# Optimization experiments

Measured on AMD Instinct MI355X. Metric: run time of the kernel, lower is better.

## Reference

```python
import jax, jax.numpy as jnp
import numpy as np

NEG_INF = -2.0**32 + 1

def positional_encoding(seq_len, dim):
    pos = np.arange(seq_len)[:, None].astype(np.float32)
    i = np.arange(dim)[None, :]
    angle_rads = pos / np.power(10000.0, 2 * (i // 2) / np.float32(dim))
    angle_rads[:, 0::2] = np.sin(angle_rads[:, 0::2])
    angle_rads[:, 1::2] = np.cos(angle_rads[:, 1::2])
    return jnp.asarray(angle_rads[None, ...], dtype=jnp.float32)  # [1, S, dim]

def setup_inputs() -> dict:
    key = jax.random.key(0)
    kq, kk, kv, km, kw = jax.random.split(key, 5)
    B, S, D = 32, 1024, 256
    return {
        'q': jax.random.normal(kq, (B, S, D), dtype=jnp.float32),
        'k': jax.random.normal(kk, (B, S, D), dtype=jnp.float32),
        'v': jax.random.normal(kv, (B, S, D), dtype=jnp.float32),
        'mask': jax.random.randint(km, (B, S), 0, 2, dtype=jnp.int32),
        'W': jax.random.uniform(kw, (D, D), dtype=jnp.float32),
    }

def reference(q, k, v, mask, W):
    B, S, D = q.shape
    pe = positional_encoding(S, D)  # [1, S, D]
    q = q + pe
    k = k + pe
    q = jax.nn.relu(jnp.matmul(q, W))
    k = jax.nn.relu(jnp.matmul(k, W))
    # scaled attention logits [B, S, S]
    logits = jnp.einsum('bqd,bkd->bqk', q, k) / jnp.sqrt(jnp.float32(D))
    m = mask[:, None, :]  # [B, 1, S], broadcasts over query dim
    logits = jnp.where(m == 0, jnp.float32(NEG_INF), logits)
    attn = jax.nn.softmax(logits, axis=-1)
    out = jnp.matmul(attn, v)          # [B, S, D]
    return jnp.mean(out, axis=1)       # [B, D]
```

## Files before the change

### kernel.cpp

```cpp
#include <hip/hip_runtime.h>

typedef float    f32x4  __attribute__((ext_vector_type(4)));
typedef float    f32x16 __attribute__((ext_vector_type(16)));
typedef _Float16 h16x8  __attribute__((ext_vector_type(8)));

#define NB 32
#define NS 1024
#define ND 256
#define NK 640
#define NEGINF (-4.2949673e9f)

__device__ __forceinline__ f32x4 mfmah(h16x8 a, h16x8 b, f32x4 c) {
    return __builtin_amdgcn_mfma_f32_16x16x32_f16(a, b, c, 0, 0, 0);
}

#define PIN(x)  asm volatile("" : "+v"(x))
#define WAITV8  asm volatile("s_waitcnt vmcnt(8)" ::: "memory")
#define WAITV0  asm volatile("s_waitcnt vmcnt(0)" ::: "memory")
#define LGKM0   asm volatile("s_waitcnt lgkmcnt(0)" ::: "memory")
#define SCHEDB  __builtin_amdgcn_sched_barrier(0)

template <typename T>
__device__ __forceinline__ void gload16(const T* g, void* l) {
    __builtin_amdgcn_global_load_lds(
        (const __attribute__((address_space(1))) void*)g,
        (__attribute__((address_space(3))) void*)l, 16, 0, 0);
}


__global__ void setup_kernel(const float* __restrict__ W, float* __restrict__ pe,
                             _Float16* __restrict__ wtt,
                             _Float16* __restrict__ wtt32) {
    int t = threadIdx.x;
    int bid = blockIdx.x;
    if (bid < 1024) {
        int s = bid, d = t;
        float f = __builtin_exp2f(-(float)(d >> 1) * 0.10381025296523007f);
        float ang = (float)s * f;
        pe[s * ND + d] = (d & 1) ? cosf(ang) : sinf(ang);
    } else if (bid < 1280) {
        int idx = (bid - 1024) * 256 + t;
        int n = idx >> 8, d = idx & 255;
        int bn = n >> 7, wn = (n >> 6) & 1, j = (n >> 4) & 3, nr = n & 15;
        int kk = d >> 5, dg = (d >> 3) & 3, e = d & 7;
        int lane = dg * 16 + nr;
        size_t off = (size_t)((((bn * 8 + kk) * 2 + wn) * 4 + j)) * 512 + lane * 8 + e;
        wtt[off] = (_Float16)W[(size_t)d * ND + n];
    } else {
        int idx = (bid - 1280) * 256 + t;
        int n = idx >> 8, d = idx & 255;
        int lane = (n & 31) + ((d >> 3) & 1) * 32;
        size_t off = (size_t)((n >> 5) * 16 + (d >> 4)) * 512 + lane * 8 + (d & 7);
        wtt32[off] = (_Float16)W[(size_t)d * ND + n];
    }
}

__global__ __launch_bounds__(256) void scan_kernel(const int* __restrict__ mask,
                                                   int* __restrict__ idxl,
                                                   int* __restrict__ cnt) {
    __shared__ int sb[256];
    int b = blockIdx.x, t = threadIdx.x;
    int m[4], psum = 0;
    #pragma unroll
    for (int e = 0; e < 4; ++e) {
        m[e] = (mask[b * 1024 + t * 4 + e] != 0) ? 1 : 0;
        psum += m[e];
    }
    sb[t] = psum;
    __syncthreads();
    #pragma unroll
    for (int off = 1; off < 256; off <<= 1) {
        int v = (t >= off) ? sb[t - off] : 0;
        __syncthreads();
        sb[t] += v;
        __syncthreads();
    }
    int excl = sb[t] - psum;
    int total = sb[255];
    int pos = excl;
    #pragma unroll
    for (int e = 0; e < 4; ++e) {
        if (m[e]) {
            if (pos < NK) idxl[b * NK + pos] = t * 4 + e;
            ++pos;
        }
    }
    if (t == 0) cnt[b] = (total > NK) ? NK : total;
    for (int p = total + t; p < NK; p += 256) idxl[b * NK + p] = 0;
}

__global__ __launch_bounds__(256, 3) void proj_kernel(
    const float* __restrict__ k, const float* __restrict__ pe,
    const _Float16* __restrict__ wtt, const int* __restrict__ idxl,
    _Float16* __restrict__ kph) {
    __shared__ __align__(16) _Float16 la[2][128][40];
    __shared__ __align__(16) _Float16 lb[2][4096];
    int t = threadIdx.x;
    int wg = blockIdx.x;
    int swz = (wg & 7) * 40 + (wg >> 3);
    int bb = swz >> 1, bn = swz & 1;
    int phase = bb & 7;
    int lane = t & 63, wid = t >> 6;
    int wm = wid >> 1, wn = wid & 1;
    int lr = lane & 15, lg = lane >> 4;

    int r0 = t >> 2, qtr0 = (t & 3) * 8;
    int r1 = 64 + (t >> 2), qtr1 = qtr0;
    int b = bb / 5, c = bb - (bb / 5) * 5;
    int o0 = idxl[b * NK + c * 128 + r0];
    int o1 = idxl[b * NK + c * 128 + r1];
    const float* aRow0 = k + ((size_t)b * 1024 + o0) * ND;
    const float* aRow1 = k + ((size_t)b * 1024 + o1) * ND;
    const float* pRow0 = pe + (size_t)o0 * ND;
    const float* pRow1 = pe + (size_t)o1 * ND;
    long destbase = (long)b * NK + c * 128;
    const _Float16* bsrc = wtt + (size_t)bn * 32768;

    f32x4 acc[4][4];
    #pragma unroll
    for (int i = 0; i < 4; ++i)
        #pragma unroll
        for (int j = 0; j < 4; ++j) acc[i][j] = (f32x4){0.f, 0.f, 0.f, 0.f};

    f32x4 ax[2][4], ap[2][4];
#define ISSUE_A(s, cc)                                                        \
    {                                                                         \
        int db_ = (cc) * 32;                                                  \
        ax[s][0] = *(const f32x4*)(aRow0 + db_ + qtr0);                       \
        ax[s][1] = *(const f32x4*)(aRow0 + db_ + qtr0 + 4);                   \
        ax[s][2] = *(const f32x4*)(aRow1 + db_ + qtr1);                       \
        ax[s][3] = *(const f32x4*)(aRow1 + db_ + qtr1 + 4);                   \
        ap[s][0] = *(const f32x4*)(pRow0 + db_ + qtr0);                       \
        ap[s][1] = *(const f32x4*)(pRow0 + db_ + qtr0 + 4);                   \
        ap[s][2] = *(const f32x4*)(pRow1 + db_ + qtr1);                       \
        ap[s][3] = *(const f32x4*)(pRow1 + db_ + qtr1 + 4);                   \
    }
#define ISSUE_B(bf, cc)                                                       \
    {                                                                         \
        const _Float16* bs_ = bsrc + (size_t)(cc) * 4096;                     \
        gload16(bs_ + t * 8, (char*)lb[bf] + t * 16);                         \
        gload16(bs_ + 2048 + t * 8, (char*)lb[bf] + 4096 + t * 16);           \
    }
    ISSUE_B(0, phase);
    ISSUE_A(0, phase);
    ISSUE_A(1, (1 + phase) & 7);

    #pragma unroll
    for (int kk = 0; kk < 8; ++kk) {
        const int buf = kk & 1;
        if (kk < 7) { WAITV8; } else { WAITV0; }
        SCHEDB;
        {
            h16x8 oA, oB;
            #pragma unroll
            for (int j = 0; j < 4; ++j) {
                oA[j]     = (_Float16)(ax[buf][0][j] + ap[buf][0][j]);
                oA[4 + j] = (_Float16)(ax[buf][1][j] + ap[buf][1][j]);
                oB[j]     = (_Float16)(ax[buf][2][j] + ap[buf][2][j]);
                oB[4 + j] = (_Float16)(ax[buf][3][j] + ap[buf][3][j]);
            }
            *(h16x8*)&la[buf][r0][qtr0] = oA;
            *(h16x8*)&la[buf][r1][qtr1] = oB;
        }
        LGKM0;
        SCHEDB;
        __builtin_amdgcn_s_barrier();
        SCHEDB;
        if (kk <= 5) {
            ISSUE_B(buf ^ 1, (kk + 1 + phase) & 7);
            ISSUE_A(buf, (kk + 2 + phase) & 7);
        } else if (kk == 6) {
            ISSUE_B(buf ^ 1, (7 + phase) & 7);
        }
        h16x8 af[4], bv[4];
        #pragma unroll
        for (int i = 0; i < 4; ++i)
            af[i] = *(const h16x8*)&la[buf][wm * 64 + i * 16 + lr][lg * 8];
        #pragma unroll
        for (int j = 0; j < 4; ++j)
            bv[j] = *(const h16x8*)((const char*)lb[buf] + (wn * 4 + j) * 1024 + lane * 16);
        #pragma unroll
        for (int i = 0; i < 4; ++i)
            #pragma unroll
            for (int j = 0; j < 4; ++j)
                acc[i][j] = mfmah(af[i], bv[j], acc[i][j]);
    }
    int nbase = bn * 128 + wn * 64;
    #pragma unroll
    for (int i = 0; i < 4; ++i) {
        #pragma unroll
        for (int jj = 0; jj < 4; ++jj) {
            long gr2 = destbase + wm * 64 + i * 16 + lg * 4 + jj;
            size_t tb = (size_t)(gr2 >> 5) * 8192 + (size_t)(gr2 & 31) * 8;
            #pragma unroll
            for (int j = 0; j < 4; ++j) {
                int col = nbase + j * 16 + lr;
                size_t off = tb + (size_t)(col >> 4) * 512
                           + (size_t)((col >> 3) & 1) * 256 + (col & 7);
                float val = acc[i][jj? j : j][jj];
                val = acc[i][j][jj];
                val = val > 0.0f ? val : 0.0f;
                kph[off] = (_Float16)val;
            }
        }
    }
}

#define STAGE_H(ldsb, hidx)                                                   \
    {                                                                         \
        const _Float16* s_ = kph + (size_t)(hidx) * 4096;                     \
        _Pragma("unroll")                                                     \
        for (int i_ = 0; i_ < 8; ++i_)                                        \
            gload16(s_ + i_ * 512 + lane * 8,                                 \
                    (char*)(ldsb) + i_ * 1024 + lane * 16);                   \
    }

#define COMPUTE_H(ldsb, pdst, fb)                                             \
    {                                                                         \
        f32x16 ao_;                                                           \
        _Pragma("unroll")                                                     \
        for (int r_ = 0; r_ < 16; ++r_) ao_[r_] = 0.f;                        \
        _Pragma("unroll")                                                     \
        for (int f_ = 0; f_ < 4; ++f_) {                                      \
            h16x8 b0_ = *(const h16x8*)((const char*)(ldsb) + (2 * f_) * 1024 + lane * 16); \
            h16x8 b1_ = *(const h16x8*)((const char*)(ldsb) + (2 * f_ + 1) * 1024 + lane * 16); \
            pdst = __builtin_amdgcn_mfma_f32_32x32x16_f16(qf[(fb) + 2 * f_], b0_, pdst, 0, 0, 0); \
            ao_  = __builtin_amdgcn_mfma_f32_32x32x16_f16(qf[(fb) + 2 * f_ + 1], b1_, ao_, 0, 0, 0); \
        }                                                                     \
        _Pragma("unroll")                                                     \
        for (int r_ = 0; r_ < 16; ++r_) pdst[r_] += ao_[r_];                  \
    }

__global__ __launch_bounds__(256, 2) void attn_kernel(
    const float* __restrict__ q, const float* __restrict__ pe,
    const _Float16* __restrict__ wtt32, const _Float16* __restrict__ kph,
    const int* __restrict__ cnt, float* __restrict__ w_part) {
    __shared__ __align__(16) char smem[66560];
    float* redm = (float*)(smem + 65536);
    float* redz = redm + 128;
    _Float16* qa_lds = (_Float16*)smem;
    _Float16* tbuf   = (_Float16*)(smem + 16384);

    int t = threadIdx.x, lane = t & 63, wid = t >> 6;
    int hi = lane >> 5, ln5 = lane & 31;
    int wg = blockIdx.x;
    int swzb = (wg & 7) * 128 + (wg >> 3);
    int b = swzb >> 5, qt = swzb & 31;

    char* buf0 = smem + wid * 16384;
    char* buf1 = buf0 + 8192;
    int hb = b * 40 + wid * 10;
    int cntb = cnt[b];

    {
        int r0 = (t * 4) & 31;
        int c8 = t >> 3;
        const float* qbase = q + ((size_t)(b * 1024 + qt * 32)) * ND + c8 * 8;
        const float* pbase = pe + (size_t)(qt * 32) * ND + c8 * 8;
        h16x8 o[4];
        #pragma unroll
        for (int e = 0; e < 4; ++e) {
            const float* s = qbase + (size_t)(r0 + e) * ND;
            const float* p = pbase + (size_t)(r0 + e) * ND;
            f32x4 x0 = *(const f32x4*)s;
            f32x4 x1 = *(const f32x4*)(s + 4);
            f32x4 p0 = *(const f32x4*)p;
            f32x4 p1 = *(const f32x4*)(p + 4);
            #pragma unroll
            for (int j = 0; j < 4; ++j) {
                o[e][j]     = (_Float16)(x0[j] + p0[j]);
                o[e][4 + j] = (_Float16)(x1[j] + p1[j]);
            }
        }
        #pragma unroll
        for (int e = 0; e < 4; ++e)
            *(h16x8*)((char*)qa_lds + t * 64 + e * 16) = o[e];
    }
    __syncthreads();
    {
        f32x16 c0, c1;
        #pragma unroll
        for (int r = 0; r < 16; ++r) { c0[r] = 0.f; c1[r] = 0.f; }
        #pragma unroll
        for (int kc = 0; kc < 16; ++kc) {
            h16x8 a = *(const h16x8*)(qa_lds + kc * 512 + lane * 8);
            h16x8 b0 = *(const h16x8*)(wtt32 + (size_t)((wid * 2) * 16 + kc) * 512 + lane * 8);
            h16x8 b1 = *(const h16x8*)(wtt32 + (size_t)((wid * 2 + 1) * 16 + kc) * 512 + lane * 8);
            c0 = __builtin_amdgcn_mfma_f32_32x32x16_f16(a, b0, c0, 0, 0, 0);
            c1 = __builtin_amdgcn_mfma_f32_32x32x16_f16(a, b1, c1, 0, 0, 0);
        }
        __syncthreads();
        #pragma unroll
        for (int r = 0; r < 16; ++r) {
            int row = (r & 3) + 8 * (r >> 2) + 4 * hi;
            int col0 = (wid * 2) * 32 + ln5;
            int col1 = (wid * 2 + 1) * 32 + ln5;
            float v0 = c0[r] > 0.f ? c0[r] : 0.f;
            float v1 = c1[r] > 0.f ? c1[r] : 0.f;
            tbuf[(col0 >> 4) * 512 + ((col0 >> 3) & 1) * 256 + row * 8 + (col0 & 7)] = (_Float16)v0;
            tbuf[(col1 >> 4) * 512 + ((col1 >> 3) & 1) * 256 + row * 8 + (col1 & 7)] = (_Float16)v1;
        }
    }
    __syncthreads();
    h16x8 qf[16];
    #pragma unroll
    for (int f = 0; f < 16; ++f)
        qf[f] = *(const h16x8*)(tbuf + f * 512 + lane * 8);
    __syncthreads();

    STAGE_H(buf0, hb + 0);
    STAGE_H(buf1, hb + 1);
    #pragma unroll
    for (int f = 0; f < 16; ++f) PIN(qf[f]);

    f32x16 p[5];
    #pragma unroll
    for (int kt = 0; kt < 5; ++kt)
        #pragma unroll
        for (int r = 0; r < 16; ++r) p[kt][r] = 0.f;

    #pragma unroll
    for (int hh = 0; hh < 10; ++hh) {
        if (hh < 9) { WAITV8; } else { WAITV0; }
        SCHEDB;
        char* bbuf = (hh & 1) ? buf1 : buf0;
        COMPUTE_H(bbuf, p[hh >> 1], (hh & 1) * 8);
        if (hh <= 7) {
            LGKM0;
            SCHEDB;
            STAGE_H(bbuf, hb + hh + 2);
        }
    }

    #pragma unroll
    for (int kt = 0; kt < 5; ++kt) {
        bool on = (wid * 160 + kt * 32 + ln5) < cntb;
        #pragma unroll
        for (int r = 0; r < 16; ++r) {
            float val = p[kt][r] * 0.0625f;
            p[kt][r] = on ? val : NEGINF;
        }
    }
    float mrow[16];
    #pragma unroll
    for (int r = 0; r < 16; ++r) {
        float m = -3.4e38f;
        #pragma unroll
        for (int kt = 0; kt < 5; ++kt) m = fmaxf(m, p[kt][r]);
        #pragma unroll
        for (int d = 1; d < 32; d <<= 1) m = fmaxf(m, __shfl_xor(m, d));
        mrow[r] = m;
    }
    if (ln5 == 0) {
        #pragma unroll
        for (int r = 0; r < 16; ++r)
            redm[wid * 32 + (r & 3) + 8 * (r >> 2) + 4 * hi] = mrow[r];
    }
    __syncthreads();
    float mf[16], zp[16];
    #pragma unroll
    for (int r = 0; r < 16; ++r) {
        int row = (r & 3) + 8 * (r >> 2) + 4 * hi;
        float m = redm[row];
        #pragma unroll
        for (int w = 1; w < 4; ++w) m = fmaxf(m, redm[w * 32 + row]);
        mf[r] = m;
        zp[r] = 0.f;
    }
    #pragma unroll
    for (int kt = 0; kt < 5; ++kt)
        #pragma unroll
        for (int r = 0; r < 16; ++r) {
            float e = __expf(p[kt][r] - mf[r]);
            p[kt][r] = e;
            zp[r] += e;
        }
    #pragma unroll
    for (int r = 0; r < 16; ++r) {
        #pragma unroll
        for (int d = 1; d < 32; d <<= 1) zp[r] += __shfl_xor(zp[r], d);
    }
    if (ln5 == 0) {
        #pragma unroll
        for (int r = 0; r < 16; ++r)
            redz[wid * 32 + (r & 3) + 8 * (r >> 2) + 4 * hi] = zp[r];
    }
    __syncthreads();
    float rz[16];
    #pragma unroll
    for (int r = 0; r < 16; ++r) {
        int row = (r & 3) + 8 * (r >> 2) + 4 * hi;
        float z = redz[row];
        #pragma unroll
        for (int w = 1; w < 4; ++w) z += redz[w * 32 + row];
        rz[r] = 1.0f / z;
    }
    float* wp = w_part + ((size_t)(b * 32 + qt)) * NK;
    #pragma unroll
    for (int kt = 0; kt < 5; ++kt) {
        float cs = 0.f;
        #pragma unroll
        for (int r = 0; r < 16; ++r) cs = fmaf(p[kt][r], rz[r], cs);
        cs += __shfl_xor(cs, 32);
        if (hi == 0) wp[wid * 160 + kt * 32 + ln5] = cs;
    }
}

__global__ void zero_out_kernel(float* __restrict__ out) {
    out[blockIdx.x * 256 + threadIdx.x] = 0.0f;
}

__global__ __launch_bounds__(256) void pv_kernel(
    const float* __restrict__ w_part, const float* __restrict__ v,
    const int* __restrict__ idxl, float* __restrict__ out) {
    __shared__ float wseg[128];
    __shared__ int sidx[128];
    int t = threadIdx.x;
    int b = blockIdx.x / 5, seg = blockIdx.x % 5;
    if (t < 128) {
        float s = 0.f;
        #pragma unroll 8
        for (int qt = 0; qt < 32; ++qt)
            s += w_part[((size_t)(b * 32 + qt)) * NK + seg * 128 + t];
        wseg[t] = s;
        sidx[t] = idxl[b * NK + seg * 128 + t];
    }
    __syncthreads();
    const float* vb = v + (size_t)b * 1024 * ND + t;
    float acc = 0.f;
    #pragma unroll 8
    for (int kk = 0; kk < 128; ++kk)
        acc = fmaf(wseg[kk], vb[(size_t)sidx[kk] * ND], acc);
    atomicAdd(out + b * 256 + t, acc * (1.0f / 1024.0f));
}

extern "C" void kernel_launch(void* const* d_in, const int* in_sizes, int n_in,
                              void* d_out, int out_size, void* d_ws, size_t ws_size,
                              hipStream_t stream) {
    const float* q = (const float*)d_in[0];
    const float* k = (const float*)d_in[1];
    const float* v = (const float*)d_in[2];
    const int* mask = (const int*)d_in[3];
    const float* W = (const float*)d_in[4];
    char* ws = (char*)d_ws;
    float*    pe    = (float*)ws;
    _Float16* wtt   = (_Float16*)(ws + 1048576);
    _Float16* wtt32 = (_Float16*)(ws + 1179648);
    int*      idxl  = (int*)(ws + 1310720);
    int*      cnt   = (int*)(ws + 1392640);
    _Float16* kph   = (_Float16*)(ws + 1441792);
    float*    wpart = (float*)(ws + 11927552);
    float* out = (float*)d_out;

    setup_kernel<<<1536, 256, 0, stream>>>(W, pe, wtt, wtt32);
    scan_kernel<<<32, 256, 0, stream>>>(mask, idxl, cnt);
    proj_kernel<<<320, 256, 0, stream>>>(k, pe, wtt, idxl, kph);
    attn_kernel<<<1024, 256, 0, stream>>>(q, pe, wtt32, kph, cnt, wpart);
    zero_out_kernel<<<32, 256, 0, stream>>>(out);
    pv_kernel<<<160, 256, 0, stream>>>(wpart, v, idxl, out);
}
```

Baseline: 78.31 us.

## Double-buffer W tiles through LDS in Q projection and coalesce Q loads

The Q-projection prologue of the attention kernel now streams W tiles into per-wave LDS double buffers with async global-to-LDS loads and explicit vmcnt waits, instead of reading them straight from global memory inside the MFMA loop. The Q+PE load is remapped so each thread reads contiguous columns of one row, which coalesces global access, and the LDS regions for Q staging move so they do not overlap the new buffers. This is meant to hide global load latency in the prologue, at the cost of extra waits and scheduling barriers. A redundant duplicate assignment in the K projection is also cleaned up.

Measured after the change: 80.06 us. 1.02x slower.

```diff
diff --git a/kernel.cpp b/kernel.cpp
--- a/kernel.cpp
+++ b/kernel.cpp
@@ -16,6 +16,7 @@
 
 #define PIN(x)  asm volatile("" : "+v"(x))
 #define WAITV8  asm volatile("s_waitcnt vmcnt(8)" ::: "memory")
+#define WAITV2  asm volatile("s_waitcnt vmcnt(2)" ::: "memory")
 #define WAITV0  asm volatile("s_waitcnt vmcnt(0)" ::: "memory")
 #define LGKM0   asm volatile("s_waitcnt lgkmcnt(0)" ::: "memory")
 #define SCHEDB  __builtin_amdgcn_sched_barrier(0)
@@ -197,8 +198,7 @@
                 int col = nbase + j * 16 + lr;
                 size_t off = tb + (size_t)(col >> 4) * 512
                            + (size_t)((col >> 3) & 1) * 256 + (col & 7);
-                float val = acc[i][jj? j : j][jj];
-                val = acc[i][j][jj];
+                float val = acc[i][j][jj];
                 val = val > 0.0f ? val : 0.0f;
                 kph[off] = (_Float16)val;
             }
@@ -238,8 +238,8 @@
     __shared__ __align__(16) char smem[66560];
     float* redm = (float*)(smem + 65536);
     float* redz = redm + 128;
-    _Float16* qa_lds = (_Float16*)smem;
-    _Float16* tbuf   = (_Float16*)(smem + 16384);
+    _Float16* qa_lds = (_Float16*)(smem + 32768);
+    _Float16* tbuf   = (_Float16*)(smem + 49152);
 
     int t = threadIdx.x, lane = t & 63, wid = t >> 6;
     int hi = lane >> 5, ln5 = lane & 31;
@@ -253,19 +253,17 @@
     int cntb = cnt[b];
 
     {
-        int r0 = (t * 4) & 31;
-        int c8 = t >> 3;
-        const float* qbase = q + ((size_t)(b * 1024 + qt * 32)) * ND + c8 * 8;
-        const float* pbase = pe + (size_t)(qt * 32) * ND + c8 * 8;
+        int row = t >> 3;
+        int cb0 = (t & 7) * 4;
+        const float* qrow = q + ((size_t)(b * 1024 + qt * 32 + row)) * ND + cb0 * 8;
+        const float* prow = pe + (size_t)(qt * 32 + row) * ND + cb0 * 8;
         h16x8 o[4];
         #pragma unroll
         for (int e = 0; e < 4; ++e) {
-            const float* s = qbase + (size_t)(r0 + e) * ND;
-            const float* p = pbase + (size_t)(r0 + e) * ND;
-            f32x4 x0 = *(const f32x4*)s;
-            f32x4 x1 = *(const f32x4*)(s + 4);
-            f32x4 p0 = *(const f32x4*)p;
-            f32x4 p1 = *(const f32x4*)(p + 4);
+            f32x4 x0 = *(const f32x4*)(qrow + e * 8);
+            f32x4 x1 = *(const f32x4*)(qrow + e * 8 + 4);
+            f32x4 p0 = *(const f32x4*)(prow + e * 8);
+            f32x4 p1 = *(const f32x4*)(prow + e * 8 + 4);
             #pragma unroll
             for (int j = 0; j < 4; ++j) {
                 o[e][j]     = (_Float16)(x0[j] + p0[j]);
@@ -274,32 +272,51 @@
         }
         #pragma unroll
         for (int e = 0; e < 4; ++e)
-            *(h16x8*)((char*)qa_lds + t * 64 + e * 16) = o[e];
-    }
-    __syncthreads();
+            *(h16x8*)(qa_lds + ((size_t)(cb0 + e) * 32 + row) * 8) = o[e];
+    }
+    __syncthreads();
+    f32x16 c0, c1;
     {
-        f32x16 c0, c1;
+        char* qpb0 = smem + wid * 8192;
+        char* qpb1 = qpb0 + 2048;
+#define FILLB(dst, kc_)                                                       \
+    {                                                                         \
+        gload16(wtt32 + (size_t)((wid * 2) * 16 + (kc_)) * 512 + lane * 8,    \
+                (dst) + lane * 16);                                           \
+        gload16(wtt32 + (size_t)((wid * 2 + 1) * 16 + (kc_)) * 512 + lane * 8,\
+                (dst) + 1024 + lane * 16);                                    \
+    }
+        FILLB(qpb0, 0);
+        FILLB(qpb1, 1);
         #pragma unroll
         for (int r = 0; r < 16; ++r) { c0[r] = 0.f; c1[r] = 0.f; }
         #pragma unroll
         for (int kc = 0; kc < 16; ++kc) {
-            h16x8 a = *(const h16x8*)(qa_lds + kc * 512 + lane * 8);
-            h16x8 b0 = *(const h16x8*)(wtt32 + (size_t)((wid * 2) * 16 + kc) * 512 + lane * 8);
-            h16x8 b1 = *(const h16x8*)(wtt32 + (size_t)((wid * 2 + 1) * 16 + kc) * 512 + lane * 8);
+            if (kc < 15) { WAITV2; } else { WAITV0; }
+            SCHEDB;
+            char* qb = (kc & 1) ? qpb1 : qpb0;
+            h16x8 a  = *(const h16x8*)(qa_lds + kc * 512 + lane * 8);
+            h16x8 b0 = *(const h16x8*)(qb + lane * 16);
+            h16x8 b1 = *(const h16x8*)(qb + 1024 + lane * 16);
             c0 = __builtin_amdgcn_mfma_f32_32x32x16_f16(a, b0, c0, 0, 0, 0);
             c1 = __builtin_amdgcn_mfma_f32_32x32x16_f16(a, b1, c1, 0, 0, 0);
-        }
-        __syncthreads();
-        #pragma unroll
-        for (int r = 0; r < 16; ++r) {
-            int row = (r & 3) + 8 * (r >> 2) + 4 * hi;
-            int col0 = (wid * 2) * 32 + ln5;
-            int col1 = (wid * 2 + 1) * 32 + ln5;
-            float v0 = c0[r] > 0.f ? c0[r] : 0.f;
-            float v1 = c1[r] > 0.f ? c1[r] : 0.f;
-            tbuf[(col0 >> 4) * 512 + ((col0 >> 3) & 1) * 256 + row * 8 + (col0 & 7)] = (_Float16)v0;
-            tbuf[(col1 >> 4) * 512 + ((col1 >> 3) & 1) * 256 + row * 8 + (col1 & 7)] = (_Float16)v1;
-        }
+            if (kc <= 13) {
+                LGKM0;
+                SCHEDB;
+                FILLB(qb, kc + 2);
+            }
+        }
+    }
+    __syncthreads();
+    #pragma unroll
+    for (int r = 0; r < 16; ++r) {
+        int row = (r & 3) + 8 * (r >> 2) + 4 * hi;
+        int col0 = (wid * 2) * 32 + ln5;
+        int col1 = (wid * 2 + 1) * 32 + ln5;
+        float v0 = c0[r] > 0.f ? c0[r] : 0.f;
+        float v1 = c1[r] > 0.f ? c1[r] : 0.f;
+        tbuf[(col0 >> 4) * 512 + ((col0 >> 3) & 1) * 256 + row * 8 + (col0 & 7)] = (_Float16)v0;
+        tbuf[(col1 >> 4) * 512 + ((col1 >> 3) & 1) * 256 + row * 8 + (col1 & 7)] = (_Float16)v1;
     }
     __syncthreads();
     h16x8 qf[16];
```

## Halve K staging tiles, stage W through LDS, and shrink shared memory

Applied to the files above, without the earlier changes.

The attention kernel now stages K in quarter-sized tiles (4 loads per stage, 20 stages), so the double buffers and shared memory drop from about 65KB to about 33KB, which may allow more resident workgroups per CU. The Q projection now streams W tiles into LDS with global_load_lds double buffering and explicit vmcnt waits, where before it read them straight from global memory. The single-chain accumulation in the logits loop replaces the dual-accumulator split. The trade-off is more pipeline stages and waits, and a longer serial MFMA dependency chain.

Result: no change. 78.17 us (-0.2%).

```diff
diff --git a/kernel.cpp b/kernel.cpp
--- a/kernel.cpp
+++ b/kernel.cpp
@@ -16,6 +16,8 @@
 
 #define PIN(x)  asm volatile("" : "+v"(x))
 #define WAITV8  asm volatile("s_waitcnt vmcnt(8)" ::: "memory")
+#define WAITV4  asm volatile("s_waitcnt vmcnt(4)" ::: "memory")
+#define WAITV2  asm volatile("s_waitcnt vmcnt(2)" ::: "memory")
 #define WAITV0  asm volatile("s_waitcnt vmcnt(0)" ::: "memory")
 #define LGKM0   asm volatile("s_waitcnt lgkmcnt(0)" ::: "memory")
 #define SCHEDB  __builtin_amdgcn_sched_barrier(0)
@@ -197,8 +199,7 @@
                 int col = nbase + j * 16 + lr;
                 size_t off = tb + (size_t)(col >> 4) * 512
                            + (size_t)((col >> 3) & 1) * 256 + (col & 7);
-                float val = acc[i][jj? j : j][jj];
-                val = acc[i][j][jj];
+                float val = acc[i][j][jj];
                 val = val > 0.0f ? val : 0.0f;
                 kph[off] = (_Float16)val;
             }
@@ -206,40 +207,24 @@
     }
 }
 
-#define STAGE_H(ldsb, hidx)                                                   \
+#define STAGE_Q(ldsb, qidx)                                                   \
     {                                                                         \
-        const _Float16* s_ = kph + (size_t)(hidx) * 4096;                     \
+        const _Float16* s_ = kph + (size_t)(qidx) * 2048;                     \
         _Pragma("unroll")                                                     \
-        for (int i_ = 0; i_ < 8; ++i_)                                        \
+        for (int i_ = 0; i_ < 4; ++i_)                                        \
             gload16(s_ + i_ * 512 + lane * 8,                                 \
                     (char*)(ldsb) + i_ * 1024 + lane * 16);                   \
-    }
-
-#define COMPUTE_H(ldsb, pdst, fb)                                             \
-    {                                                                         \
-        f32x16 ao_;                                                           \
-        _Pragma("unroll")                                                     \
-        for (int r_ = 0; r_ < 16; ++r_) ao_[r_] = 0.f;                        \
-        _Pragma("unroll")                                                     \
-        for (int f_ = 0; f_ < 4; ++f_) {                                      \
-            h16x8 b0_ = *(const h16x8*)((const char*)(ldsb) + (2 * f_) * 1024 + lane * 16); \
-            h16x8 b1_ = *(const h16x8*)((const char*)(ldsb) + (2 * f_ + 1) * 1024 + lane * 16); \
-            pdst = __builtin_amdgcn_mfma_f32_32x32x16_f16(qf[(fb) + 2 * f_], b0_, pdst, 0, 0, 0); \
-            ao_  = __builtin_amdgcn_mfma_f32_32x32x16_f16(qf[(fb) + 2 * f_ + 1], b1_, ao_, 0, 0, 0); \
-        }                                                                     \
-        _Pragma("unroll")                                                     \
-        for (int r_ = 0; r_ < 16; ++r_) pdst[r_] += ao_[r_];                  \
     }
 
 __global__ __launch_bounds__(256, 2) void attn_kernel(
     const float* __restrict__ q, const float* __restrict__ pe,
     const _Float16* __restrict__ wtt32, const _Float16* __restrict__ kph,
     const int* __restrict__ cnt, float* __restrict__ w_part) {
-    __shared__ __align__(16) char smem[66560];
-    float* redm = (float*)(smem + 65536);
+    __shared__ __align__(16) char smem[33792];
+    float* redm = (float*)(smem + 32768);
     float* redz = redm + 128;
     _Float16* qa_lds = (_Float16*)smem;
-    _Float16* tbuf   = (_Float16*)(smem + 16384);
+    _Float16* tbuf   = (_Float16*)smem;
 
     int t = threadIdx.x, lane = t & 63, wid = t >> 6;
     int hi = lane >> 5, ln5 = lane & 31;
@@ -247,9 +232,9 @@
     int swzb = (wg & 7) * 128 + (wg >> 3);
     int b = swzb >> 5, qt = swzb & 31;
 
-    char* buf0 = smem + wid * 16384;
-    char* buf1 = buf0 + 8192;
-    int hb = b * 40 + wid * 10;
+    char* buf0 = smem + wid * 8192;
+    char* buf1 = buf0 + 4096;
+    int qb = b * 80 + wid * 20;
     int cntb = cnt[b];
 
     {
@@ -277,29 +262,48 @@
             *(h16x8*)((char*)qa_lds + t * 64 + e * 16) = o[e];
     }
     __syncthreads();
+    f32x16 c0, c1;
     {
-        f32x16 c0, c1;
+        char* qpb0 = smem + 16384 + wid * 4096;
+        char* qpb1 = qpb0 + 2048;
+#define FILLB(dst, kc_)                                                       \
+    {                                                                         \
+        gload16(wtt32 + (size_t)((wid * 2) * 16 + (kc_)) * 512 + lane * 8,    \
+                (dst) + lane * 16);                                           \
+        gload16(wtt32 + (size_t)((wid * 2 + 1) * 16 + (kc_)) * 512 + lane * 8,\
+                (dst) + 1024 + lane * 16);                                    \
+    }
+        FILLB(qpb0, 0);
+        FILLB(qpb1, 1);
         #pragma unroll
         for (int r = 0; r < 16; ++r) { c0[r] = 0.f; c1[r] = 0.f; }
         #pragma unroll
         for (int kc = 0; kc < 16; ++kc) {
-            h16x8 a = *(const h16x8*)(qa_lds + kc * 512 + lane * 8);
-            h16x8 b0 = *(const h16x8*)(wtt32 + (size_t)((wid * 2) * 16 + kc) * 512 + lane * 8);
-            h16x8 b1 = *(const h16x8*)(wtt32 + (size_t)((wid * 2 + 1) * 16 + kc) * 512 + lane * 8);
+            if (kc < 15) { WAITV2; } else { WAITV0; }
+            SCHEDB;
+            char* qbp = (kc & 1) ? qpb1 : qpb0;
+            h16x8 a  = *(const h16x8*)(qa_lds + kc * 512 + lane * 8);
+            h16x8 b0 = *(const h16x8*)(qbp + lane * 16);
+            h16x8 b1 = *(const h16x8*)(qbp + 1024 + lane * 16);
             c0 = __builtin_amdgcn_mfma_f32_32x32x16_f16(a, b0, c0, 0, 0, 0);
             c1 = __builtin_amdgcn_mfma_f32_32x32x16_f16(a, b1, c1, 0, 0, 0);
-        }
-        __syncthreads();
-        #pragma unroll
-        for (int r = 0; r < 16; ++r) {
-            int row = (r & 3) + 8 * (r >> 2) + 4 * hi;
-            int col0 = (wid * 2) * 32 + ln5;
-            int col1 = (wid * 2 + 1) * 32 + ln5;
-            float v0 = c0[r] > 0.f ? c0[r] : 0.f;
-            float v1 = c1[r] > 0.f ? c1[r] : 0.f;
-            tbuf[(col0 >> 4) * 512 + ((col0 >> 3) & 1) * 256 + row * 8 + (col0 & 7)] = (_Float16)v0;
-            tbuf[(col1 >> 4) * 512 + ((col1 >> 3) & 1) * 256 + row * 8 + (col1 & 7)] = (_Float16)v1;
-        }
+            if (kc <= 13) {
+                LGKM0;
+                SCHEDB;
+                FILLB(qbp, kc + 2);
+            }
+        }
+    }
+    __syncthreads();
+    #pragma unroll
+    for (int r = 0; r < 16; ++r) {
+        int row = (r & 3) + 8 * (r >> 2) + 4 * hi;
+        int col0 = (wid * 2) * 32 + ln5;
+        int col1 = (wid * 2 + 1) * 32 + ln5;
+        float v0 = c0[r] > 0.f ? c0[r] : 0.f;
+        float v1 = c1[r] > 0.f ? c1[r] : 0.f;
+        tbuf[(col0 >> 4) * 512 + ((col0 >> 3) & 1) * 256 + row * 8 + (col0 & 7)] = (_Float16)v0;
+        tbuf[(col1 >> 4) * 512 + ((col1 >> 3) & 1) * 256 + row * 8 + (col1 & 7)] = (_Float16)v1;
     }
     __syncthreads();
     h16x8 qf[16];
@@ -308,8 +312,8 @@
         qf[f] = *(const h16x8*)(tbuf + f * 512 + lane * 8);
     __syncthreads();
 
-    STAGE_H(buf0, hb + 0);
-    STAGE_H(buf1, hb + 1);
+    STAGE_Q(buf0, qb + 0);
+    STAGE_Q(buf1, qb + 1);
     #pragma unroll
     for (int f = 0; f < 16; ++f) PIN(qf[f]);
 
@@ -320,15 +324,24 @@
         for (int r = 0; r < 16; ++r) p[kt][r] = 0.f;
 
     #pragma unroll
-    for (int hh = 0; hh < 10; ++hh) {
-        if (hh < 9) { WAITV8; } else { WAITV0; }
+    for (int s = 0; s < 20; ++s) {
+        if (s < 19) { WAITV4; } else { WAITV0; }
         SCHEDB;
-        char* bbuf = (hh & 1) ? buf1 : buf0;
-        COMPUTE_H(bbuf, p[hh >> 1], (hh & 1) * 8);
-        if (hh <= 7) {
+        char* bb = (s & 1) ? buf1 : buf0;
+        {
+            h16x8 b0 = *(const h16x8*)(bb + lane * 16);
+            h16x8 b1 = *(const h16x8*)(bb + 1024 + lane * 16);
+            h16x8 b2 = *(const h16x8*)(bb + 2048 + lane * 16);
+            h16x8 b3 = *(const h16x8*)(bb + 3072 + lane * 16);
+            p[s >> 2] = __builtin_amdgcn_mfma_f32_32x32x16_f16(qf[(s & 3) * 4 + 0], b0, p[s >> 2], 0, 0, 0);
+            p[s >> 2] = __builtin_amdgcn_mfma_f32_32x32x16_f16(qf[(s & 3) * 4 + 1], b1, p[s >> 2], 0, 0, 0);
+            p[s >> 2] = __builtin_amdgcn_mfma_f32_32x32x16_f16(qf[(s & 3) * 4 + 2], b2, p[s >> 2], 0, 0, 0);
+            p[s >> 2] = __builtin_amdgcn_mfma_f32_32x32x16_f16(qf[(s & 3) * 4 + 3], b3, p[s >> 2], 0, 0, 0);
+        }
+        if (s <= 17) {
             LGKM0;
             SCHEDB;
-            STAGE_H(bbuf, hb + hh + 2);
+            STAGE_Q(bb, qb + s + 2);
         }
     }
 
```
